# Kernel tuning notes

Hardware: AMD Instinct MI355X
Metric: run time of the kernel (lower is better)

The kernel has to match this reference:

```python
import jax, jax.numpy as jnp
import numpy as np

OUT_CHANNELS = 16
PH = PW = 7          # output_size
SR = 2               # sampling_ratio


def setup_inputs() -> dict:
    key = jax.random.key(0)
    k1, k2, k3, k4 = jax.random.split(key, 4)
    B, C, H, W = 4, OUT_CHANNELS * PH * PW, 80, 80
    feat = jax.random.normal(k1, (B, C, H, W), dtype=jnp.float32)
    N = 512
    bidx = jax.random.randint(k2, (N,), 0, B).astype(jnp.float32)
    tl = jax.random.uniform(k3, (N, 2), minval=0.0, maxval=0.7)   # x1, y1 (normalized)
    sz = jax.random.uniform(k4, (N, 2), minval=0.05, maxval=0.3)  # box size
    rois = jnp.concatenate([bidx[:, None], tl, tl + sz], axis=1)  # [N,5]
    return {"input": feat, "rois": rois}


def _psroi_one(feat_ps, roi):
    # feat_ps: [B, Co, PH, PW, H, W]  (position-sensitive channel layout)
    B, Co, _, _, H, W = feat_ps.shape
    f = feat_ps[roi[0].astype(jnp.int32)]              # [Co, PH, PW, H, W]
    x1 = roi[1] * W; y1 = roi[2] * H
    x2 = roi[3] * W; y2 = roi[4] * H                   # adaptive spatial_scale = (H, W)
    roi_h = jnp.maximum(y2 - y1, 0.1)
    roi_w = jnp.maximum(x2 - x1, 0.1)
    bin_h = roi_h / PH
    bin_w = roi_w / PW
    # sample coordinates per bin: [PH,SR] and [PW,SR]
    ys = y1 + jnp.arange(PH, dtype=f.dtype)[:, None] * bin_h + (jnp.arange(SR, dtype=f.dtype)[None, :] + 0.5) * bin_h / SR
    xs = x1 + jnp.arange(PW, dtype=f.dtype)[:, None] * bin_w + (jnp.arange(SR, dtype=f.dtype)[None, :] + 0.5) * bin_w / SR
    ym = (ys >= -1.0) & (ys <= H)
    xm = (xs >= -1.0) & (xs <= W)
    yc = jnp.clip(ys, 0.0, H - 1)
    xc = jnp.clip(xs, 0.0, W - 1)
    y0 = jnp.floor(yc).astype(jnp.int32)
    x0 = jnp.floor(xc).astype(jnp.int32)
    y1i = jnp.minimum(y0 + 1, H - 1)
    x1i = jnp.minimum(x0 + 1, W - 1)
    ly = yc - y0.astype(f.dtype); hy = 1.0 - ly        # [PH,SR]
    lx = xc - x0.astype(f.dtype); hx = 1.0 - lx        # [PW,SR]
    I = jnp.arange(PH)[:, None, None, None]            # bin row index
    J = jnp.arange(PW)[None, None, :, None]            # bin col index

    def g(Y, X):
        # gather f[c, i, j, Y[i,sy], X[j,sx]] -> [Co, PH, SR, PW, SR]
        return f[:, I, J, Y[:, :, None, None], X[None, None, :, :]]

    v = (g(y0, x0)  * (hy[:, :, None, None] * hx[None, None])
       + g(y0, x1i) * (hy[:, :, None, None] * lx[None, None])
       + g(y1i, x0) * (ly[:, :, None, None] * hx[None, None])
       + g(y1i, x1i) * (ly[:, :, None, None] * lx[None, None]))
    v = v * (ym[:, :, None, None] & xm[None, None]).astype(v.dtype)
    return v.mean(axis=(2, 4))                          # [Co, PH, PW]


def reference(input, rois):
    B, C, H, W = input.shape
    feat_ps = input.reshape(B, OUT_CHANNELS, PH, PW, H, W)
    rois = rois.reshape(-1, 5)
    out = jax.vmap(lambda r: _psroi_one(feat_ps, r))(rois)  # [N, Co, PH, PW]
    return out
```

## Files before the change

kernel.cpp:

```cpp
#include <hip/hip_runtime.h>

#define NB   4
#define CO   16
#define PH   7
#define PW   7
#define SR   2
#define HH   80
#define WW   80
#define NROI 512
#define CIJ  (CO*PH*PW)
#define PLANE (HH*WW)
#define NF4  (PLANE/4)

typedef float f4v __attribute__((ext_vector_type(4), aligned(16)));

__global__ __launch_bounds__(512, 8) void psroi_align_kernel(
    const float* __restrict__ feat,
    const float* __restrict__ rois,
    float* __restrict__ out)
{
    __shared__ __align__(16) float sp[PLANE];
    __shared__ unsigned short order[NROI];
    __shared__ int cnt[NB];
    __shared__ int base[NB + 1];

    int cij = blockIdx.x;
    int rem = cij % (PH * PW);
    int i = rem / PW;
    int j = rem % PW;
    int n = threadIdx.x;

    if (n < NB) cnt[n] = 0;
    __syncthreads();
    int myb = (int)rois[n * 5 + 0];
    int rank = atomicAdd(&cnt[myb], 1);
    __syncthreads();
    if (n == 0) {
        base[0] = 0;
        for (int k = 0; k < NB; ++k) base[k + 1] = base[k] + cnt[k];
    }
    __syncthreads();
    order[base[myb] + rank] = (unsigned short)n;

    f4v regs[4];
    {
        const f4v* src = (const f4v*)(feat + (size_t)cij * PLANE);
        #pragma unroll
        for (int it = 0; it < 4; ++it) {
            int e = it * 512 + n;
            if (e < NF4) regs[it] = src[e];
        }
        #pragma unroll
        for (int it = 0; it < 4; ++it) {
            int e = it * 512 + n;
            if (e < NF4) ((f4v*)sp)[e] = regs[it];
        }
    }

    for (int bb = 0; bb < NB; ++bb) {
        if (bb + 1 < NB) {
            const f4v* src = (const f4v*)(feat + ((size_t)(bb + 1) * CIJ + cij) * PLANE);
            #pragma unroll
            for (int it = 0; it < 4; ++it) {
                int e = it * 512 + n;
                if (e < NF4) regs[it] = src[e];
            }
        }
        __syncthreads();

        if (n >= base[bb] && n < base[bb + 1]) {
            int m = order[n];
            float x1 = rois[m * 5 + 1] * (float)WW;
            float y1 = rois[m * 5 + 2] * (float)HH;
            float x2 = rois[m * 5 + 3] * (float)WW;
            float y2 = rois[m * 5 + 4] * (float)HH;
            float bin_h = fmaxf(y2 - y1, 0.1f) * (1.0f / PH);
            float bin_w = fmaxf(x2 - x1, 0.1f) * (1.0f / PW);

            float acc = 0.0f;
            #pragma unroll
            for (int sy = 0; sy < SR; ++sy) {
                float ys = y1 + (float)i * bin_h + ((float)sy + 0.5f) * bin_h / (float)SR;
                bool ymask = (ys >= -1.0f) && (ys <= (float)HH);
                float yc = fminf(fmaxf(ys, 0.0f), (float)(HH - 1));
                int   y0 = (int)floorf(yc);
                int   y1i = min(y0 + 1, HH - 1);
                float ly = yc - (float)y0, hy = 1.0f - ly;
                #pragma unroll
                for (int sx = 0; sx < SR; ++sx) {
                    float xs = x1 + (float)j * bin_w + ((float)sx + 0.5f) * bin_w / (float)SR;
                    bool xmask = (xs >= -1.0f) && (xs <= (float)WW);
                    float xc = fminf(fmaxf(xs, 0.0f), (float)(WW - 1));
                    int   x0 = (int)floorf(xc);
                    int   x0c = min(x0, WW - 2);
                    bool  sh = (x0 != x0c);
                    float lx = xc - (float)x0, hx = 1.0f - lx;

                    float t0 = sp[y0  * WW + x0c], t1 = sp[y0  * WW + x0c + 1];
                    float b0 = sp[y1i * WW + x0c], b1 = sp[y1i * WW + x0c + 1];

                    float v00 = sh ? t1 : t0;
                    float v10 = sh ? b1 : b0;
                    float v = (v00 * hx + t1 * lx) * hy + (v10 * hx + b1 * lx) * ly;
                    if (ymask && xmask) acc += v;
                }
            }
            out[(size_t)m * CIJ + cij] = acc * 0.25f;
        }

        if (bb + 1 < NB) {
            __syncthreads();
            #pragma unroll
            for (int it = 0; it < 4; ++it) {
                int e = it * 512 + n;
                if (e < NF4) ((f4v*)sp)[e] = regs[it];
            }
        }
    }
}

extern "C" void kernel_launch(void* const* d_in, const int* in_sizes, int n_in,
                              void* d_out, int out_size, void* d_ws, size_t ws_size,
                              hipStream_t stream)
{
    const float* feat = (const float*)d_in[0];
    const float* rois = (const float*)d_in[1];
    float* out = (float*)d_out;

    psroi_align_kernel<<<CIJ, NROI, 0, stream>>>(feat, rois, out);
}
```

Measured before the change: 114.2 us.

## Split ROI sorting into prep kernel and parallelize main kernel over batch

Adds a single-block prep kernel that buckets ROIs by batch index and precomputes per-ROI box geometry into the workspace. The main kernel now launches one 256-thread block per (channel, batch) pair instead of one 512-thread block looping over all four batches. Each block loads only its own feature plane and processes only the ROIs of that batch. This removes the sequential batch loop, the per-block redundant sort, and most idle threads, but it adds a second launch and a dependency through global memory.

```diff
diff --git a/kernel.cpp b/kernel.cpp
--- a/kernel.cpp
+++ b/kernel.cpp
@@ -14,108 +14,108 @@
 
 typedef float f4v __attribute__((ext_vector_type(4), aligned(16)));
 
-__global__ __launch_bounds__(512, 8) void psroi_align_kernel(
+#define WS_ORDER_OFF 64
+#define WS_GEOM_OFF  2048
+
+__global__ __launch_bounds__(512) void psroi_prep_kernel(
+    const float* __restrict__ rois, int* __restrict__ base,
+    unsigned short* __restrict__ order, f4v* __restrict__ geom)
+{
+    __shared__ int cnt[NB];
+    __shared__ int cbase[NB + 1];
+    int n = threadIdx.x;
+    if (n < NB) cnt[n] = 0;
+    __syncthreads();
+    int b = (int)rois[n * 5 + 0];
+    int rank = atomicAdd(&cnt[b], 1);
+    __syncthreads();
+    if (n == 0) {
+        cbase[0] = 0;
+        for (int k = 0; k < NB; ++k) cbase[k + 1] = cbase[k] + cnt[k];
+        for (int k = 0; k <= NB; ++k) base[k] = cbase[k];
+    }
+    __syncthreads();
+    int pos = cbase[b] + rank;
+    order[pos] = (unsigned short)n;
+
+    float x1 = rois[n * 5 + 1] * (float)WW;
+    float y1 = rois[n * 5 + 2] * (float)HH;
+    float x2 = rois[n * 5 + 3] * (float)WW;
+    float y2 = rois[n * 5 + 4] * (float)HH;
+    f4v g;
+    g.x = x1;
+    g.y = y1;
+    g.z = fmaxf(x2 - x1, 0.1f) * (1.0f / PW);
+    g.w = fmaxf(y2 - y1, 0.1f) * (1.0f / PH);
+    geom[pos] = g;
+}
+
+__global__ __launch_bounds__(256) void psroi_main_kernel(
     const float* __restrict__ feat,
-    const float* __restrict__ rois,
+    const int* __restrict__ base,
+    const unsigned short* __restrict__ order,
+    const f4v* __restrict__ geom,
     float* __restrict__ out)
 {
     __shared__ __align__(16) float sp[PLANE];
-    __shared__ unsigned short order[NROI];
-    __shared__ int cnt[NB];
-    __shared__ int base[NB + 1];
 
-    int cij = blockIdx.x;
+    int u   = blockIdx.x;
+    int cij = u >> 2;
+    int b   = u & 3;
     int rem = cij % (PH * PW);
     int i = rem / PW;
     int j = rem % PW;
     int n = threadIdx.x;
 
-    if (n < NB) cnt[n] = 0;
-    __syncthreads();
-    int myb = (int)rois[n * 5 + 0];
-    int rank = atomicAdd(&cnt[myb], 1);
-    __syncthreads();
-    if (n == 0) {
-        base[0] = 0;
-        for (int k = 0; k < NB; ++k) base[k + 1] = base[k] + cnt[k];
-    }
-    __syncthreads();
-    order[base[myb] + rank] = (unsigned short)n;
-
-    f4v regs[4];
+    const f4v* src = (const f4v*)(feat + ((size_t)b * CIJ + (size_t)cij) * PLANE);
+    f4v* dst = (f4v*)sp;
+    #pragma unroll
+    for (int it = 0; it < 6; ++it)
+        dst[it * 256 + n] = src[it * 256 + n];
     {
-        const f4v* src = (const f4v*)(feat + (size_t)cij * PLANE);
-        #pragma unroll
-        for (int it = 0; it < 4; ++it) {
-            int e = it * 512 + n;
-            if (e < NF4) regs[it] = src[e];
-        }
-        #pragma unroll
-        for (int it = 0; it < 4; ++it) {
-            int e = it * 512 + n;
-            if (e < NF4) ((f4v*)sp)[e] = regs[it];
-        }
+        int e = 1536 + n;
+        if (e < NF4) dst[e] = src[e];
     }
 
-    for (int bb = 0; bb < NB; ++bb) {
-        if (bb + 1 < NB) {
-            const f4v* src = (const f4v*)(feat + ((size_t)(bb + 1) * CIJ + cij) * PLANE);
+    int lo = base[b];
+    int hi = base[b + 1];
+
+    __syncthreads();
+
+    for (int t = lo + n; t < hi; t += 256) {
+        int m = (int)order[t];
+        f4v g = geom[t];
+        float x1 = g.x, y1 = g.y, bin_w = g.z, bin_h = g.w;
+
+        float acc = 0.0f;
+        #pragma unroll
+        for (int sy = 0; sy < SR; ++sy) {
+            float ys = y1 + (float)i * bin_h + ((float)sy + 0.5f) * bin_h / (float)SR;
+            bool ymask = (ys >= -1.0f) && (ys <= (float)HH);
+            float yc = fminf(fmaxf(ys, 0.0f), (float)(HH - 1));
+            int   y0 = (int)floorf(yc);
+            int   y1i = min(y0 + 1, HH - 1);
+            float ly = yc - (float)y0, hy = 1.0f - ly;
             #pragma unroll
-            for (int it = 0; it < 4; ++it) {
-                int e = it * 512 + n;
-                if (e < NF4) regs[it] = src[e];
+            for (int sx = 0; sx < SR; ++sx) {
+                float xs = x1 + (float)j * bin_w + ((float)sx + 0.5f) * bin_w / (float)SR;
+                bool xmask = (xs >= -1.0f) && (xs <= (float)WW);
+                float xc = fminf(fmaxf(xs, 0.0f), (float)(WW - 1));
+                int   x0 = (int)floorf(xc);
+                int   x0c = min(x0, WW - 2);
+                bool  sh = (x0 != x0c);
+                float lx = xc - (float)x0, hx = 1.0f - lx;
+
+                float t0 = sp[y0  * WW + x0c], t1 = sp[y0  * WW + x0c + 1];
+                float b0 = sp[y1i * WW + x0c], b1 = sp[y1i * WW + x0c + 1];
+
+                float v00 = sh ? t1 : t0;
+                float v10 = sh ? b1 : b0;
+                float v = (v00 * hx + t1 * lx) * hy + (v10 * hx + b1 * lx) * ly;
+                if (ymask && xmask) acc += v;
             }
         }
-        __syncthreads();
-
-        if (n >= base[bb] && n < base[bb + 1]) {
-            int m = order[n];
-            float x1 = rois[m * 5 + 1] * (float)WW;
-            float y1 = rois[m * 5 + 2] * (float)HH;
-            float x2 = rois[m * 5 + 3] * (float)WW;
-            float y2 = rois[m * 5 + 4] * (float)HH;
-            float bin_h = fmaxf(y2 - y1, 0.1f) * (1.0f / PH);
-            float bin_w = fmaxf(x2 - x1, 0.1f) * (1.0f / PW);
-
-            float acc = 0.0f;
-            #pragma unroll
-            for (int sy = 0; sy < SR; ++sy) {
-                float ys = y1 + (float)i * bin_h + ((float)sy + 0.5f) * bin_h / (float)SR;
-                bool ymask = (ys >= -1.0f) && (ys <= (float)HH);
-                float yc = fminf(fmaxf(ys, 0.0f), (float)(HH - 1));
-                int   y0 = (int)floorf(yc);
-                int   y1i = min(y0 + 1, HH - 1);
-                float ly = yc - (float)y0, hy = 1.0f - ly;
-                #pragma unroll
-                for (int sx = 0; sx < SR; ++sx) {
-                    float xs = x1 + (float)j * bin_w + ((float)sx + 0.5f) * bin_w / (float)SR;
-                    bool xmask = (xs >= -1.0f) && (xs <= (float)WW);
-                    float xc = fminf(fmaxf(xs, 0.0f), (float)(WW - 1));
-                    int   x0 = (int)floorf(xc);
-                    int   x0c = min(x0, WW - 2);
-                    bool  sh = (x0 != x0c);
-                    float lx = xc - (float)x0, hx = 1.0f - lx;
-
-                    float t0 = sp[y0  * WW + x0c], t1 = sp[y0  * WW + x0c + 1];
-                    float b0 = sp[y1i * WW + x0c], b1 = sp[y1i * WW + x0c + 1];
-
-                    float v00 = sh ? t1 : t0;
-                    float v10 = sh ? b1 : b0;
-                    float v = (v00 * hx + t1 * lx) * hy + (v10 * hx + b1 * lx) * ly;
-                    if (ymask && xmask) acc += v;
-                }
-            }
-            out[(size_t)m * CIJ + cij] = acc * 0.25f;
-        }
-
-        if (bb + 1 < NB) {
-            __syncthreads();
-            #pragma unroll
-            for (int it = 0; it < 4; ++it) {
-                int e = it * 512 + n;
-                if (e < NF4) ((f4v*)sp)[e] = regs[it];
-            }
-        }
+        out[(size_t)m * CIJ + cij] = acc * 0.25f;
     }
 }
 
@@ -127,5 +127,11 @@
     const float* rois = (const float*)d_in[1];
     float* out = (float*)d_out;
 
-    psroi_align_kernel<<<CIJ, NROI, 0, stream>>>(feat, rois, out);
+    char* ws = (char*)d_ws;
+    int* base = (int*)ws;
+    unsigned short* order = (unsigned short*)(ws + WS_ORDER_OFF);
+    f4v* geom = (f4v*)(ws + WS_GEOM_OFF);
+
+    psroi_prep_kernel<<<1, NROI, 0, stream>>>(rois, base, order, geom);
+    psroi_main_kernel<<<CIJ * NB, 256, 0, stream>>>(feat, base, order, geom, out);
 }
```

Result: faster. 111.3 us (-2.5%).
